# Performance work log

Measured on AMD Instinct MI355X. Metric: run time of the kernel, lower is better.

## Reference

```python
import jax, jax.numpy as jnp
import numpy as np

B, V, D = 4096, 20, 768


def _conv1d_k3(x, w, b):
    # x: [B, V, D]; single-channel conv1d, kernel=3, padding=1 (torch cross-correlation)
    xp = jnp.pad(x, ((0, 0), (0, 0), (1, 1)))
    return w[0] * xp[..., :-2] + w[1] * xp[..., 1:-1] + w[2] * xp[..., 2:] + b[0]


def setup_inputs() -> dict:
    key = jax.random.key(0)
    ks = jax.random.split(key, 10)
    s = 0.02  # small init scale for weights
    return {
        "text_features": jax.random.normal(ks[0], (B, D), jnp.float32),
        "viewport_features": jax.random.normal(ks[1], (B, V, D), jnp.float32),
        "W1": jax.random.normal(ks[2], (D, D), jnp.float32) * s,
        "b1": jax.random.normal(ks[3], (D,), jnp.float32) * s,
        "W2": jax.random.normal(ks[4], (D, D), jnp.float32) * s,
        "b2": jax.random.normal(ks[5], (D,), jnp.float32) * s,
        "cw1": jax.random.normal(ks[6], (3,), jnp.float32) * 0.5,
        "cb1": jax.random.normal(ks[7], (1,), jnp.float32) * 0.1,
        "cw2": jax.random.normal(ks[8], (3,), jnp.float32) * 0.5,
        "cb2": jax.random.normal(ks[9], (1,), jnp.float32) * 0.1,
    }


def reference(text_features, viewport_features, W1, b1, W2, b2, cw1, cb1, cw2, cb2):
    # Batched over all 20 viewports at once (original loops over i).
    fli_norm = jax.nn.softmax(viewport_features, axis=-1)          # [B,V,D]
    # torch Linear: x @ W.T + b
    m1 = jnp.einsum('bvd,ed->bve', fli_norm, W1) + b1              # mlp1(fli_norm)
    m2 = jnp.einsum('bvd,ed->bve', fli_norm, W2) + b2              # mlp2(fli_norm)
    fused = jax.nn.relu(text_features[:, None, :] * m1 + m2)       # [B,V,D]
    fused = _conv1d_k3(fused, cw1, cb1)
    fused = jax.nn.relu(fused)
    fused = _conv1d_k3(fused, cw2, cb2)
    return fused.reshape(B, V * D)                                 # torch.cat along dim=1
```

## Files before the change

kernel.cpp:

```cpp
#include <hip/hip_runtime.h>

typedef unsigned short u16;
typedef unsigned char u8;
typedef __attribute__((ext_vector_type(8))) short short8;
typedef __attribute__((ext_vector_type(4))) float f32x4;

#define Bn 4096
#define Vn 20
#define Dn 768
#define Mn (Bn * Vn)
#define Nn (2 * Dn)

#define BM 256
#define BNt 256
#define NTILES (Nn / BNt)
#define GRID ((Mn / BM) * NTILES)
#define PANEL (256 * Dn)

#define SCL 32.0f
#define ISCL2 (1.0f / 1024.0f)

typedef __attribute__((address_space(1))) void GV;
typedef __attribute__((address_space(3))) void LV;

__device__ __forceinline__ u16 f2bf(float f) {
  union { float f; unsigned u; } v; v.f = f;
  unsigned r = v.u + 0x7FFFu + ((v.u >> 16) & 1u);
  return (u16)(r >> 16);
}
__device__ __forceinline__ float bf2f(u16 x) {
  union { unsigned u; float f; } v; v.u = ((unsigned)x) << 16; return v.f;
}


__global__ __launch_bounds__(192) void softmax_k(const float* __restrict__ vf,
                                                 u8* __restrict__ X8) {
  size_t row = blockIdx.x;
  const float4* p = (const float4*)(vf + row * Dn);
  int t = threadIdx.x;
  float4 v = p[t];
  float mx = fmaxf(fmaxf(v.x, v.y), fmaxf(v.z, v.w));
  #pragma unroll
  for (int off = 32; off; off >>= 1) mx = fmaxf(mx, __shfl_xor(mx, off));
  __shared__ float rr[3];
  __shared__ float rs[3];
  int wv = t >> 6, ln = t & 63;
  if (!ln) rr[wv] = mx;
  __syncthreads();
  mx = fmaxf(fmaxf(rr[0], rr[1]), rr[2]);
  float e0 = __expf(v.x - mx), e1 = __expf(v.y - mx);
  float e2 = __expf(v.z - mx), e3 = __expf(v.w - mx);
  float s = e0 + e1 + e2 + e3;
  #pragma unroll
  for (int off = 32; off; off >>= 1) s += __shfl_xor(s, off);
  if (!ln) rs[wv] = s;
  __syncthreads();
  float inv = SCL / (rs[0] + rs[1] + rs[2]);
  unsigned pk = 0;
  pk = __builtin_amdgcn_cvt_pk_fp8_f32(e0 * inv, e1 * inv, pk, false);
  pk = __builtin_amdgcn_cvt_pk_fp8_f32(e2 * inv, e3 * inv, pk, true);
  const int q = (int)(row & 255);
  u8* dst = X8 + (row >> 8) * PANEL + (size_t)(t >> 3) * 8192
            + ((t >> 1) & 3) * 2048 + (q >> 1) * 16 + (q & 1) * 8 + (t & 1) * 4;
  *(unsigned*)dst = pk;
}

__global__ __launch_bounds__(256) void build_wt_k(const float* __restrict__ W1,
                                                  const float* __restrict__ W2,
                                                  u8* __restrict__ Wt8) {
  int idx = blockIdx.x * 256 + threadIdx.x;
  if (idx >= Dn * (Dn / 4)) return;
  int j = idx / (Dn / 4), d4 = (idx - j * (Dn / 4)) * 4;
  int b = j >> 5, c = j & 31;
  float4 a = *(const float4*)(W1 + (size_t)j * Dn + d4);
  float4 e = *(const float4*)(W2 + (size_t)j * Dn + d4);
  unsigned p1 = 0, p2 = 0;
  p1 = __builtin_amdgcn_cvt_pk_fp8_f32(a.x * SCL, a.y * SCL, p1, false);
  p1 = __builtin_amdgcn_cvt_pk_fp8_f32(a.z * SCL, a.w * SCL, p1, true);
  p2 = __builtin_amdgcn_cvt_pk_fp8_f32(e.x * SCL, e.y * SCL, p2, false);
  p2 = __builtin_amdgcn_cvt_pk_fp8_f32(e.z * SCL, e.w * SCL, p2, true);
  const int slice = d4 >> 5, plane = (d4 >> 3) & 3, bb = d4 & 7;
  const int j1 = b * 64 + c, j2 = b * 64 + 32 + c;
  const int q1 = j1 & 255, q2 = j2 & 255;
  *(unsigned*)(Wt8 + (size_t)(j1 >> 8) * PANEL + (size_t)slice * 8192
               + plane * 2048 + (q1 >> 1) * 16 + (q1 & 1) * 8 + bb) = p1;
  *(unsigned*)(Wt8 + (size_t)(j2 >> 8) * PANEL + (size_t)slice * 8192
               + plane * 2048 + (q2 >> 1) * 16 + (q2 & 1) * 8 + bb) = p2;
}

__global__ __launch_bounds__(512, 2) void gemm_fuse_k(
    const u8* __restrict__ X8, const u8* __restrict__ Wt8,
    const float* __restrict__ b1, const float* __restrict__ b2,
    const float* __restrict__ text, float* __restrict__ out,
    u16* __restrict__ seam,
    const float* __restrict__ cw1, const float* __restrict__ cb1,
    const float* __restrict__ cw2, const float* __restrict__ cb2) {
  __shared__ __align__(16) u16 smem[65536];
  u8* smem8 = (u8*)smem;

  const int h = blockIdx.x;
  const int lin = (h & 7) * (GRID / 8) + (h >> 3);
  const int by = lin / NTILES, bx = lin - by * NTILES;
  const int brow = by * BM;

  const int t = threadIdx.x, w = t >> 6, l = t & 63;
  const int lo = l & 15, hi = l >> 4;
  const int wrr = w >> 2, wcc = w & 3;

  int offA[8], offB[4];
  #pragma unroll
  for (int m = 0; m < 8; ++m)
    offA[m] = hi * 2048 + (wrr * 64 + m * 8 + (lo >> 1)) * 16 + (lo & 1) * 8;
  #pragma unroll
  for (int n = 0; n < 4; ++n)
    offB[n] = hi * 2048 + (wcc * 32 + n * 8 + (lo >> 1)) * 16 + (lo & 1) * 8;

  const u8* gAp = X8 + (size_t)by * PANEL + t * 16;
  const u8* gBp = Wt8 + (size_t)bx * PANEL + t * 16;

#define STG_A(DST, SL) __builtin_amdgcn_global_load_lds( \
    (GV*)(gAp + (size_t)(SL) * 8192), (LV*)(smem8 + (DST) + w * 1024), 16, 0, 0)
#define STG_B(DST, SL) __builtin_amdgcn_global_load_lds( \
    (GV*)(gBp + (size_t)(SL) * 8192), (LV*)(smem8 + (DST) + w * 1024), 16, 0, 0)

  STG_A(0, 0);              STG_B(16384, 0);
  STG_A(32768, 2);          STG_B(49152, 2);
  STG_A(8192, 1);           STG_B(24576, 1);
  STG_A(40960, 3);          STG_B(57344, 3);
  asm volatile("s_waitcnt vmcnt(6)" ::: "memory");
  __builtin_amdgcn_s_barrier();

  f32x4 acc[8][4] = {};
  long af[8], bb0, bb1;

#define PH(SB, KH, NH, NEWA, STG, VM) do {                                     \
    if (NEWA) { _Pragma("unroll") for (int m = 0; m < 8; ++m)                  \
      af[m] = *(const long*)(smem8 + (SB) + (KH) * 8192 + offA[m]); }          \
    bb0 = *(const long*)(smem8 + (SB) + 16384 + (KH) * 8192 + offB[(NH)*2]);   \
    bb1 = *(const long*)(smem8 + (SB) + 16384 + (KH) * 8192 + offB[(NH)*2+1]); \
    STG;                                                                       \
    __builtin_amdgcn_s_barrier();                                              \
    asm volatile("s_waitcnt lgkmcnt(0)" ::: "memory");                         \
    __builtin_amdgcn_sched_barrier(0);                                         \
    __builtin_amdgcn_s_setprio(1);                                             \
    _Pragma("unroll") for (int m = 0; m < 8; ++m) {                            \
      acc[m][(NH)*2]   = __builtin_amdgcn_mfma_f32_16x16x32_fp8_fp8(af[m], bb0, acc[m][(NH)*2],   0, 0, 0); \
      acc[m][(NH)*2+1] = __builtin_amdgcn_mfma_f32_16x16x32_fp8_fp8(af[m], bb1, acc[m][(NH)*2+1], 0, 0, 0); \
    }                                                                          \
    __builtin_amdgcn_s_setprio(0);                                             \
    VM;                                                                        \
    __builtin_amdgcn_s_barrier();                                              \
  } while (0)

#define VM2 asm volatile("s_waitcnt vmcnt(2)" ::: "memory")
#define VM0 asm volatile("s_waitcnt vmcnt(0)" ::: "memory")

  #pragma unroll
  for (int i = 0; i < 6; ++i) {
    const int sa = 2 * (2 * i + 1);
    const int sb = 2 * (2 * i + 2);
    PH(0, 0, 0, true,  if (i >= 1) STG_A(32768, sa),     ;  );
    PH(0, 0, 1, false, if (i >= 1) STG_B(49152, sa),     VM2);
    PH(0, 1, 0, true,  if (i >= 1) STG_A(40960, sa + 1), ;  );
    PH(0, 1, 1, false, if (i >= 1) STG_B(57344, sa + 1), VM2);
    PH(32768, 0, 0, true,  if (i <= 4) STG_A(0, sb),         ;  );
    PH(32768, 0, 1, false, if (i <= 4) STG_B(16384, sb),     if (i == 5) { VM0; } else { VM2; });
    PH(32768, 1, 0, true,  if (i <= 4) STG_A(8192, sb + 1),  ;  );
    PH(32768, 1, 1, false, if (i <= 4) STG_B(24576, sb + 1), if (i <= 4) { VM2; });
  }
#undef PH
#undef VM2
#undef VM0
#undef STG_A
#undef STG_B

  const float w10 = cw1[0], w11 = cw1[1], w12 = cw1[2], c1b = cb1[0];
  const float w20 = cw2[0], w21 = cw2[1], w22 = cw2[2], c2b = cb2[0];

  u16* fsm = smem;
  u16* tsm = smem + 32768;

  #pragma unroll
  for (int n = 0; n < 2; ++n) {
    const int cl = wcc * 32 + n * 16 + lo;
    const int e  = bx * 128 + cl;
    const float B1 = b1[e], B2 = b2[e];
    #pragma unroll
    for (int m = 0; m < 8; ++m) {
      const int rl = wrr * 128 + m * 16 + hi * 4;
      uint2 pk;
      u16* pku = (u16*)&pk;
      #pragma unroll
      for (int r = 0; r < 4; ++r) {
        const int gr = brow + rl + r;
        const float v1 = acc[m][n][r] * ISCL2 + B1;
        const float v2 = acc[m][n + 2][r] * ISCL2 + B2;
        const float tf = text[(size_t)(gr / Vn) * Dn + e];
        pku[r] = f2bf(fmaxf(tf * v1 + v2, 0.0f));
      }
      *(uint2*)(fsm + cl * 256 + (rl ^ ((cl & 31) << 3))) = pk;
      const int sidx = (cl < 4) ? cl : ((cl >= 124) ? cl - 120 : -1);
      if (sidx >= 0)
        *(uint2*)(seam + ((size_t)(by * 6 + bx) * 8 + sidx) * 256 + rl) = pk;
    }
  }
  __syncthreads();

  const int cl = t & 127, rb = t >> 7;
  const int cL = cl ? cl - 1 : 0, cR = (cl < 127) ? cl + 1 : 127;
  short8 tC[8];
  #pragma unroll
  for (int j = 0; j < 8; ++j) {
    const int R = rb * 64 + j * 8;
    short8 sL = *(const short8*)(fsm + cL * 256 + (R ^ ((cL & 31) << 3)));
    short8 sC = *(const short8*)(fsm + cl * 256 + (R ^ ((cl & 31) << 3)));
    short8 sR = *(const short8*)(fsm + cR * 256 + (R ^ ((cR & 31) << 3)));
    short8 o;
    #pragma unroll
    for (int k = 0; k < 8; ++k) {
      float a = bf2f((u16)sL[k]), b = bf2f((u16)sC[k]), c = bf2f((u16)sR[k]);
      float v = fmaxf(fmaf(w10, a, fmaf(w11, b, fmaf(w12, c, c1b))), 0.0f);
      o[k] = (short)f2bf(v);
    }
    *(short8*)(tsm + cl * 256 + (R ^ ((cl & 31) << 3))) = o;
    tC[j] = o;
  }
  __syncthreads();

  const bool wr_ok = (cl >= 2 && cl <= 125);
  #pragma unroll
  for (int j = 0; j < 8; ++j) {
    const int R = rb * 64 + j * 8;
    short8 tL = *(const short8*)(tsm + cL * 256 + (R ^ ((cL & 31) << 3)));
    short8 tR = *(const short8*)(tsm + cR * 256 + (R ^ ((cR & 31) << 3)));
    #pragma unroll
    for (int k = 0; k < 8; ++k) {
      float v = fmaf(w20, bf2f((u16)tL[k]),
                fmaf(w21, bf2f((u16)tC[j][k]),
                fmaf(w22, bf2f((u16)tR[k]), c2b)));
      if (wr_ok)
        out[(size_t)(brow + R + k) * Dn + bx * 128 + cl] = v;
    }
  }
}

__global__ __launch_bounds__(256) void seam_k(const u16* __restrict__ seam,
                                              float* __restrict__ out,
                                              const float* __restrict__ cw1,
                                              const float* __restrict__ cb1,
                                              const float* __restrict__ cw2,
                                              const float* __restrict__ cb2) {
  const int bid = blockIdx.x;
  const int by = bid / 6, bx = bid - by * 6;
  const int r = threadIdx.x;
  const float w10 = cw1[0], w11 = cw1[1], w12 = cw1[2], c1b = cb1[0];
  const float w20 = cw2[0], w21 = cw2[1], w22 = cw2[2], c2b = cb2[0];
  #define SM(B, I) bf2f(seam[((size_t)(B) * 8 + (I)) * 256 + r])
  float fm2 = 0.f, fm1 = 0.f, fR0 = 0.f, fR1 = 0.f;
  if (bx > 0) { fm2 = SM(bid - 1, 6); fm1 = SM(bid - 1, 7); }
  if (bx < 5) { fR0 = SM(bid + 1, 0); fR1 = SM(bid + 1, 1); }
  const float f0 = SM(bid, 0), f1 = SM(bid, 1), f2 = SM(bid, 2), f3 = SM(bid, 3);
  const float f124 = SM(bid, 4), f125 = SM(bid, 5), f126 = SM(bid, 6), f127 = SM(bid, 7);
  #undef SM
  #define C1(a, b, c) fmaxf(fmaf(w10, (a), fmaf(w11, (b), fmaf(w12, (c), c1b))), 0.0f)
  const float tm1  = (bx > 0) ? C1(fm2, fm1, f0) : 0.0f;
  const float t0   = C1(fm1, f0, f1);
  const float t1   = C1(f0, f1, f2);
  const float t2   = C1(f1, f2, f3);
  const float t125 = C1(f124, f125, f126);
  const float t126 = C1(f125, f126, f127);
  const float t127 = C1(f126, f127, fR0);
  const float t128 = (bx < 5) ? C1(f127, fR0, fR1) : 0.0f;
  #undef C1
  const size_t go = (size_t)(by * 256 + r) * Dn + bx * 128;
  out[go + 0]   = fmaf(w20, tm1,  fmaf(w21, t0,   fmaf(w22, t1,   c2b)));
  out[go + 1]   = fmaf(w20, t0,   fmaf(w21, t1,   fmaf(w22, t2,   c2b)));
  out[go + 126] = fmaf(w20, t125, fmaf(w21, t126, fmaf(w22, t127, c2b)));
  out[go + 127] = fmaf(w20, t126, fmaf(w21, t127, fmaf(w22, t128, c2b)));
}

extern "C" void kernel_launch(void* const* d_in, const int* in_sizes, int n_in,
                              void* d_out, int out_size, void* d_ws, size_t ws_size,
                              hipStream_t stream) {
  const float* text = (const float*)d_in[0];
  const float* vf   = (const float*)d_in[1];
  const float* W1   = (const float*)d_in[2];
  const float* b1   = (const float*)d_in[3];
  const float* W2   = (const float*)d_in[4];
  const float* b2   = (const float*)d_in[5];
  const float* cw1  = (const float*)d_in[6];
  const float* cb1  = (const float*)d_in[7];
  const float* cw2  = (const float*)d_in[8];
  const float* cb2  = (const float*)d_in[9];
  float* out = (float*)d_out;

  u8*  X8   = (u8*)d_ws;
  u8*  Wt8  = X8 + (size_t)Mn * Dn;
  u16* seam = (u16*)(Wt8 + (size_t)Nn * Dn);

  softmax_k<<<Mn, 192, 0, stream>>>(vf, X8);
  build_wt_k<<<(Dn * (Dn / 4) + 255) / 256, 256, 0, stream>>>(W1, W2, Wt8);
  gemm_fuse_k<<<GRID, 512, 0, stream>>>(X8, Wt8, b1, b2, text, out, seam,
                                        cw1, cb1, cw2, cb2);
  seam_k<<<GRID, 256, 0, stream>>>(seam, out, cw1, cb1, cw2, cb2);
}
```

Baseline: 375.7 us.

## Process 32 softmax rows per block and stage FP8 output through LDS

The softmax kernel now handles 32 rows per 512-thread block, with 16 threads per row, so reductions use only intra-wave shuffles and no shared-memory round trip or barriers. The FP8 results are assembled in LDS in the panel layout the GEMM expects, then written out with coalesced 16-byte stores instead of scattered 4-byte stores. This cuts launch count and global write inefficiency, at the cost of more registers per thread (12 float4) and 24KB of LDS per block.

```diff
diff --git a/kernel.cpp b/kernel.cpp
--- a/kernel.cpp
+++ b/kernel.cpp
@@ -33,36 +33,49 @@
 }
 
 
-__global__ __launch_bounds__(192) void softmax_k(const float* __restrict__ vf,
+__global__ __launch_bounds__(512) void softmax_k(const float* __restrict__ vf,
                                                  u8* __restrict__ X8) {
-  size_t row = blockIdx.x;
-  const float4* p = (const float4*)(vf + row * Dn);
-  int t = threadIdx.x;
-  float4 v = p[t];
-  float mx = fmaxf(fmaxf(v.x, v.y), fmaxf(v.z, v.w));
-  #pragma unroll
-  for (int off = 32; off; off >>= 1) mx = fmaxf(mx, __shfl_xor(mx, off));
-  __shared__ float rr[3];
-  __shared__ float rs[3];
-  int wv = t >> 6, ln = t & 63;
-  if (!ln) rr[wv] = mx;
+  __shared__ __align__(16) u8 lds[24576];
+  const int t = threadIdx.x;
+  const int r = t >> 4;
+  const int g = t & 15;
+  const size_t q = (size_t)blockIdx.x * 32 + r;
+  const float* src = vf + q * Dn + g * 4;
+  float4 v[12];
+  #pragma unroll
+  for (int u = 0; u < 12; ++u) v[u] = *(const float4*)(src + u * 64);
+  float mx = -1e30f;
+  #pragma unroll
+  for (int u = 0; u < 12; ++u)
+    mx = fmaxf(mx, fmaxf(fmaxf(v[u].x, v[u].y), fmaxf(v[u].z, v[u].w)));
+  #pragma unroll
+  for (int off = 1; off < 16; off <<= 1) mx = fmaxf(mx, __shfl_xor(mx, off));
+  float s = 0.f;
+  #pragma unroll
+  for (int u = 0; u < 12; ++u) {
+    v[u].x = __expf(v[u].x - mx); v[u].y = __expf(v[u].y - mx);
+    v[u].z = __expf(v[u].z - mx); v[u].w = __expf(v[u].w - mx);
+    s += (v[u].x + v[u].y) + (v[u].z + v[u].w);
+  }
+  #pragma unroll
+  for (int off = 1; off < 16; off <<= 1) s += __shfl_xor(s, off);
+  const float inv = SCL / s;
+  const int base = ((g >> 1) & 3) * 256 + (r >> 1) * 16 + (r & 1) * 8 + (g & 1) * 4;
+  #pragma unroll
+  for (int u = 0; u < 12; ++u) {
+    unsigned pk = 0;
+    pk = __builtin_amdgcn_cvt_pk_fp8_f32(v[u].x * inv, v[u].y * inv, pk, false);
+    pk = __builtin_amdgcn_cvt_pk_fp8_f32(v[u].z * inv, v[u].w * inv, pk, true);
+    *(unsigned*)(lds + ((g >> 3) + 2 * u) * 1024 + base) = pk;
+  }
   __syncthreads();
-  mx = fmaxf(fmaxf(rr[0], rr[1]), rr[2]);
-  float e0 = __expf(v.x - mx), e1 = __expf(v.y - mx);
-  float e2 = __expf(v.z - mx), e3 = __expf(v.w - mx);
-  float s = e0 + e1 + e2 + e3;
-  #pragma unroll
-  for (int off = 32; off; off >>= 1) s += __shfl_xor(s, off);
-  if (!ln) rs[wv] = s;
-  __syncthreads();
-  float inv = SCL / (rs[0] + rs[1] + rs[2]);
-  unsigned pk = 0;
-  pk = __builtin_amdgcn_cvt_pk_fp8_f32(e0 * inv, e1 * inv, pk, false);
-  pk = __builtin_amdgcn_cvt_pk_fp8_f32(e2 * inv, e3 * inv, pk, true);
-  const int q = (int)(row & 255);
-  u8* dst = X8 + (row >> 8) * PANEL + (size_t)(t >> 3) * 8192
-            + ((t >> 1) & 3) * 2048 + (q >> 1) * 16 + (q & 1) * 8 + (t & 1) * 4;
-  *(unsigned*)dst = pk;
+  u8* dst = X8 + (size_t)(blockIdx.x >> 3) * PANEL + (blockIdx.x & 7) * 256;
+  #pragma unroll
+  for (int rd = 0; rd < 3; ++rd) {
+    const int o = (rd * 512 + t) * 16;
+    *(uint4*)(dst + (o >> 10) * 8192 + ((o >> 8) & 3) * 2048 + (o & 255)) =
+        *(const uint4*)(lds + o);
+  }
 }
 
 __global__ __launch_bounds__(256) void build_wt_k(const float* __restrict__ W1,
@@ -298,7 +311,7 @@
   u8*  Wt8  = X8 + (size_t)Mn * Dn;
   u16* seam = (u16*)(Wt8 + (size_t)Nn * Dn);
 
-  softmax_k<<<Mn, 192, 0, stream>>>(vf, X8);
+  softmax_k<<<Mn / 32, 512, 0, stream>>>(vf, X8);
   build_wt_k<<<(Dn * (Dn / 4) + 255) / 256, 256, 0, stream>>>(W1, W2, Wt8);
   gemm_fuse_k<<<GRID, 512, 0, stream>>>(X8, Wt8, b1, b2, text, out, seam,
                                         cw1, cb1, cw2, cb2);
```

Result: faster. 336.9 us (-10.3%).
